# Optimization experiments

Hardware: AMD Instinct MI355X
Metric: run time of the kernel (lower is better)

The kernel has to match this reference:

```python
import jax, jax.numpy as jnp
import numpy as np

B, NN, D = 16, 50, 400
H, DH = 20, 20
ATT_H = 128
NEWS = 20000
K = 10
STEPS, SLOTS = 6, 10
EPS = 1e-5


def _layer_norm(x, g, b):
    m = jnp.mean(x, -1, keepdims=True)
    v = jnp.mean(jnp.square(x - m), -1, keepdims=True)
    return (x - m) * jax.lax.rsqrt(v + EPS) * g + b


def setup_inputs():
    key = jax.random.key(0)
    ks = jax.random.split(key, 9)
    s = 1.0 / np.sqrt(D)
    return {
        "news_input": jax.random.normal(ks[0], (B, NN, D), jnp.float32),
        "outputs_table": jax.random.normal(ks[1], (NEWS, K, D), jnp.float32) * 0.1,
        "Wq": jax.random.normal(ks[2], (D, H * DH), jnp.float32) * s,
        "Wk": jax.random.normal(ks[3], (D, H * DH), jnp.float32) * s,
        "Wv": jax.random.normal(ks[4], (D, H * DH), jnp.float32) * s,
        "ln1_g": jnp.ones((D,), jnp.float32),
        "ln1_b": jnp.zeros((D,), jnp.float32),
        "fc1_w": jax.random.normal(ks[5], (D, ATT_H), jnp.float32) * s,
        "fc1_b": jnp.zeros((ATT_H,), jnp.float32),
        "fc2_w": jax.random.normal(ks[6], (ATT_H, 1), jnp.float32) * (1.0 / np.sqrt(ATT_H)),
        "fc2_b": jnp.zeros((1,), jnp.float32),
        "ln2_g": jnp.ones((D,), jnp.float32),
        "ln2_b": jnp.zeros((D,), jnp.float32),
        "click_history": jax.random.randint(ks[7], (B, NN), 1, NEWS + 1),
        "neighbor_table": jax.random.randint(ks[8], (NEWS + 1, K), 1, NEWS + 1),
        "mask": jnp.ones((B, 50 * SLOTS), jnp.int32),
    }


def _traverse(news_input, outputs_table, click_history, neighbor_table):
    # Vectorized form of the per-item 6-hop neighbor traversal.
    def step(carry, _):
        idx, dead = carry                                          # [B,N] int, [B,N] bool
        vg = outputs_table[idx - 1]                                # [B,N,K,D] gather
        scores = jnp.einsum('bnkd,bnd->bnk', vg, news_input)      # [B,N,K]
        mx_i = jnp.argmax(scores, -1)
        mx_v = jnp.take_along_axis(scores, mx_i[..., None], -1)[..., 0]
        nz = scores != 0
        any_nz = jnp.any(nz, -1)
        nz_i = jnp.argmax(jnp.where(nz, scores, -jnp.inf), -1)
        hop = (mx_v == 0) & jnp.logical_not(dead)                  # max score exactly 0 -> follow graph
        sel_i = jnp.where(hop & any_nz, nz_i, mx_i)
        new_dead = dead | (hop & jnp.logical_not(any_nz))
        nbr = jnp.take_along_axis(neighbor_table[idx], sel_i[..., None], -1)[..., 0]
        new_idx = jnp.where(hop & any_nz, nbr, idx)
        sel = jnp.take_along_axis(vg, sel_i[..., None, None], 2)[..., 0, :]
        sel = jnp.where(new_dead[..., None], 0.0, sel)
        return (new_idx, new_dead), sel

    init = (click_history, jnp.zeros(click_history.shape, bool))
    _, sels = jax.lax.scan(step, init, None, length=STEPS)         # [6,B,N,D]
    sels = jnp.moveaxis(sels, 0, 2)                                # [B,N,6,D]
    valid = jnp.any(news_input != 0, -1).astype(sels.dtype)        # skip all-zero news rows
    sels = sels * valid[..., None, None]
    res = jnp.pad(sels, ((0, 0), (0, 0), (0, SLOTS - STEPS), (0, 0)))
    if NN < 50:
        res = jnp.pad(res, ((0, 0), (0, 50 - NN), (0, 0), (0, 0)))
    return res                                                      # [B,50,10,D]


def _mha(x, mask, Wq, Wk, Wv):
    L = x.shape[1]
    q = (x @ Wq).reshape(-1, L, H, DH).transpose(0, 2, 1, 3)
    k = (x @ Wk).reshape(-1, L, H, DH).transpose(0, 2, 1, 3)
    v = (x @ Wv).reshape(-1, L, H, DH).transpose(0, 2, 1, 3)
    sc = jnp.einsum('bhqd,bhkd->bhqk', q, k) / np.float32(np.sqrt(DH))
    sc = jnp.where(mask[:, None, None, :] > 0, sc, -1e9)
    a = jax.nn.softmax(sc, -1)
    o = jnp.einsum('bhqk,bhkd->bhqd', a, v)
    return o.transpose(0, 2, 1, 3).reshape(-1, L, H * DH)


def _att_pool(x, mask, fc1_w, fc1_b, fc2_w, fc2_b):
    e = jnp.tanh(x @ fc1_w + fc1_b) @ fc2_w + fc2_b                # [B*50,10,1]
    e = jnp.where(mask[..., None] > 0, e, -1e9)
    a = jax.nn.softmax(e, 1)
    return jnp.sum(a * x, 1)


def reference(news_input, outputs_table, Wq, Wk, Wv, ln1_g, ln1_b,
              fc1_w, fc1_b, fc2_w, fc2_b, ln2_g, ln2_b,
              click_history, neighbor_table, mask):
    res = _traverse(news_input, outputs_table, click_history, neighbor_table)
    x = res.reshape(-1, 50 * SLOTS, D)
    x = _mha(x, mask, Wq, Wk, Wv)
    x = x.reshape(-1, SLOTS, D)
    x = _layer_norm(x, ln1_g, ln1_b)
    x = _att_pool(x, mask.reshape(-1, SLOTS), fc1_w, fc1_b, fc2_w, fc2_b)
    x = _layer_norm(x, ln2_g, ln2_b)
    return x.reshape(-1, 50, D)
```

## Files before the change

kernel.cpp:

```cpp
#include <hip/hip_runtime.h>
#include <hip/hip_bf16.h>
#include <math.h>

#define B 16
#define NN 50
#define D 400
#define H 20
#define DH 20
#define ATT_H 128
#define NEWS 20000
#define K 10
#define STEPS 6
#define SLOTS 10
#define L 500
#define EPS 1e-5f

#define XP 416
#define NC 1200

typedef short short4v __attribute__((ext_vector_type(4)));
typedef short short8 __attribute__((ext_vector_type(8)));
typedef float floatx4 __attribute__((ext_vector_type(4)));

__device__ __forceinline__ short f2bf(float f) {
    __hip_bfloat16 h = __float2bfloat16(f);
    return *reinterpret_cast<short*>(&h);
}

__global__ __launch_bounds__(256) void k_traverse(
    const float* __restrict__ news,
    const float* __restrict__ table,
    const int*   __restrict__ click,
    const int*   __restrict__ nbrt,
    short* __restrict__ x)
{
    __shared__ float ssc[K];

    int item = blockIdx.x;
    int b = item / NN, n = item % NN;
    int tid = threadIdx.x;
    int lane = tid & 63, w = tid >> 6;

    float nv[7];
    bool nzf = false;
    #pragma unroll
    for (int i = 0; i < 7; i++) {
        int d = lane + 64 * i;
        float v = (d < D) ? news[(size_t)item * D + d] : 0.0f;
        nv[i] = v;
        nzf |= (v != 0.0f);
    }
    float valid = __any(nzf) ? 1.0f : 0.0f;

    int idx = click[item];
    bool dead = false;
    short* xbase = x + (size_t)(b * L + n * SLOTS) * XP;

    for (int step = 0; step < STEPS; step++) {
        const float* tb = table + (size_t)(idx - 1) * K * D;
        for (int kk = w; kk < K; kk += 4) {
            float p = 0.0f;
            #pragma unroll
            for (int i = 0; i < 7; i++) {
                int d = lane + 64 * i;
                if (d < D) p += tb[kk * D + d] * nv[i];
            }
            #pragma unroll
            for (int off = 32; off > 0; off >>= 1) p += __shfl_xor(p, off);
            if (lane == 0) ssc[kk] = p;
        }
        __syncthreads();

        float scores[K];
        #pragma unroll
        for (int kk = 0; kk < K; kk++) scores[kk] = ssc[kk];

        int mx_i = 0; float mx_v = scores[0];
        #pragma unroll
        for (int kk = 1; kk < K; kk++)
            if (scores[kk] > mx_v) { mx_v = scores[kk]; mx_i = kk; }

        bool any_nz = false; int nz_i = 0; float nz_v = -INFINITY;
        #pragma unroll
        for (int kk = 0; kk < K; kk++) {
            if (scores[kk] != 0.0f) {
                if (!any_nz || scores[kk] > nz_v) { nz_v = scores[kk]; nz_i = kk; }
                any_nz = true;
            }
        }

        bool hop = (mx_v == 0.0f) && !dead;
        int sel_i = (hop && any_nz) ? nz_i : mx_i;
        bool new_dead = dead || (hop && !any_nz);
        int nbr = nbrt[(size_t)idx * K + sel_i];
        int new_idx = (hop && any_nz) ? nbr : idx;

        float scale = new_dead ? 0.0f : valid;
        const float* selrow = tb + (size_t)sel_i * D;
        short* xr = xbase + (size_t)step * XP;
        for (int d = tid; d < XP; d += 256)
            xr[d] = (d < D) ? f2bf(selrow[d] * scale) : (short)0;

        idx = new_idx; dead = new_dead;
        __syncthreads();
    }
    for (int s = STEPS; s < SLOTS; s++) {
        short* xr = xbase + (size_t)s * XP;
        for (int d = tid; d < XP; d += 256) xr[d] = 0;
    }
}

__global__ __launch_bounds__(256) void k_wconvT(
    const float* __restrict__ Wq, const float* __restrict__ Wk,
    const float* __restrict__ Wv, short* __restrict__ wT)
{
    int c = blockIdx.x;
    int z = c / 400, n = c % 400;
    const float* W = (z == 0) ? Wq : (z == 1) ? Wk : Wv;
    for (int k = threadIdx.x; k < XP; k += 256)
        wT[(size_t)c * XP + k] = (k < 400) ? f2bf(W[(size_t)k * 400 + n]) : (short)0;
}

#define BM 128
#define BN 64
#define BKK 32

__global__ __launch_bounds__(256) void k_qkv_mfma(
    const short* __restrict__ xg,
    const short* __restrict__ wT,
    float* __restrict__ c)
{
    __shared__ short xs[BM][BKK + 8];
    __shared__ short wt[BN][BKK + 8];

    int tid = threadIdx.x;
    int m0 = blockIdx.x * BM;
    int n0 = blockIdx.y * BN;
    int lane = tid & 63, w = tid >> 6;
    int wr = w >> 1, wc = w & 1;
    int quad = lane >> 4, l16 = lane & 15;

    floatx4 acc[4][2];
    #pragma unroll
    for (int i = 0; i < 4; i++)
        #pragma unroll
        for (int j = 0; j < 2; j++) acc[i][j] = (floatx4){0.f, 0.f, 0.f, 0.f};

    int xr = tid >> 1, xc = (tid & 1) * 16;
    int wrow = tid >> 2, wcol8 = (tid & 3) * 8;
    bool xok = (m0 + xr) < 8000;
    bool wok = (n0 + wrow) < NC;

    for (int k0 = 0; k0 < XP; k0 += BKK) {
        int4 xv0 = {0,0,0,0}, xv1 = {0,0,0,0}, wv = {0,0,0,0};
        if (xok) {
            const int4* src = (const int4*)(xg + (size_t)(m0 + xr) * XP + k0 + xc);
            xv0 = src[0]; xv1 = src[1];
        }
        if (wok)
            wv = *(const int4*)(wT + (size_t)(n0 + wrow) * XP + k0 + wcol8);
        __syncthreads();
        *(int4*)&xs[xr][xc]      = xv0;
        *(int4*)&xs[xr][xc + 8]  = xv1;
        *(int4*)&wt[wrow][wcol8] = wv;
        __syncthreads();

        short8 a[4], bf[2];
        #pragma unroll
        for (int fi = 0; fi < 4; fi++)
            a[fi] = *(const short8*)&xs[wr * 64 + fi * 16 + l16][quad * 8];
        #pragma unroll
        for (int fj = 0; fj < 2; fj++)
            bf[fj] = *(const short8*)&wt[wc * 32 + fj * 16 + l16][quad * 8];
        #pragma unroll
        for (int fi = 0; fi < 4; fi++)
            #pragma unroll
            for (int fj = 0; fj < 2; fj++)
                acc[fi][fj] = __builtin_amdgcn_mfma_f32_16x16x32_bf16(
                    a[fi], bf[fj], acc[fi][fj], 0, 0, 0);
    }

    #pragma unroll
    for (int fi = 0; fi < 4; fi++) {
        int grow_base = m0 + wr * 64 + fi * 16 + quad * 4;
        #pragma unroll
        for (int fj = 0; fj < 2; fj++) {
            int gcol = n0 + wc * 32 + fj * 16 + l16;
            #pragma unroll
            for (int r = 0; r < 4; r++) {
                int grow = grow_base + r;
                if (grow < 8000 && gcol < NC)
                    c[(size_t)grow * NC + gcol] = acc[fi][fj][r];
            }
        }
    }
}

#define KSTR 24
#define VSTR 520
#define PSTR 40
#define QSPLIT 4

__global__ __launch_bounds__(256) void k_attn4(
    const float* __restrict__ qkv,
    const int* __restrict__ mask,
    float* __restrict__ o)
{
    __shared__ short sh[12288 + 21 * VSTR + 4 * 16 * PSTR + 512];
    short* VTb = sh + 12288;
    short* Pb  = VTb + 21 * VSTR;
    short* msk = Pb + 4 * 16 * PSTR;

    int part = blockIdx.x & (QSPLIT - 1);
    int bh = blockIdx.x >> 2;
    int b = bh / H, h = bh % H;
    int tid = threadIdx.x;
    int lane = tid & 63, w = tid >> 6;
    int quad = lane >> 4, l16 = lane & 15;
    const float scale = 0.22360679774997896f;

    for (int i = tid; i < 512 * KSTR; i += 256) {
        int j = i / KSTR, d = i % KSTR;
        float v = (j < L && d < DH) ? qkv[(size_t)(b * L + j) * NC + 400 + h * DH + d] : 0.0f;
        sh[i] = f2bf(v);
    }
    for (int i = tid; i < L * DH; i += 256) {
        int j = i / DH, d = i % DH;
        VTb[d * VSTR + j] = f2bf(qkv[(size_t)(b * L + j) * NC + 800 + h * DH + d]);
    }
    for (int j = tid; j < 512; j += 256) {
        VTb[20 * VSTR + j] = (j < L) ? f2bf(1.0f) : (short)0;
        msk[j] = (j < L && mask[(size_t)b * L + j] > 0) ? f2bf(1.0f) : (short)0;
    }
    for (int i = tid; i < DH * 12; i += 256) {
        int d = i / 12, j = L + i % 12;
        VTb[d * VSTR + j] = 0;
    }
    __syncthreads();

    short* Pw = Pb + w * 16 * PSTR;
    short* pwr = Pw + l16 * PSTR;
    const short* prd = Pw + l16 * PSTR + quad * 8;
    const short* kA  = sh + quad * 8;
    const short* vA0 = VTb + l16 * VSTR;
    int r1 = 16 + l16; if (r1 > 20) r1 = 20;
    const short* vA1 = VTb + r1 * VSTR;

    for (int qt = part * 8 + w; qt < part * 8 + 8; qt += 4) {
        int qrow = qt * 16 + l16;
        const float* qp = qkv + (size_t)(b * L + (qrow < L ? qrow : 0)) * NC + h * DH;
        short8 aq;
        #pragma unroll
        for (int jj = 0; jj < 8; jj++) {
            int k = quad * 8 + jj;
            float v = (k < DH) ? qp[k] * scale : 0.0f;
            aq[jj] = f2bf(v);
        }

        floatx4 O0 = (floatx4){0.f,0.f,0.f,0.f};
        floatx4 O1 = (floatx4){0.f,0.f,0.f,0.f};
        float mrun = -INFINITY;

        for (int jt = 0; jt < 16; jt++) {
            short8 ak0 = (short8)(short)0, ak1 = (short8)(short)0;
            if (quad < 3) {
                ak0 = *(const short8*)&kA[(jt * 32 + l16) * KSTR];
                ak1 = *(const short8*)&kA[(jt * 32 + 16 + l16) * KSTR];
            }
            floatx4 z = (floatx4){0.f,0.f,0.f,0.f};
            floatx4 s0 = __builtin_amdgcn_mfma_f32_16x16x32_bf16(ak0, aq, z, 0, 0, 0);
            floatx4 s1 = __builtin_amdgcn_mfma_f32_16x16x32_bf16(ak1, aq, z, 0, 0, 0);

            short4v mk0 = *(const short4v*)&msk[jt * 32 + quad * 4];
            short4v mk1 = *(const short4v*)&msk[jt * 32 + 16 + quad * 4];
            #pragma unroll
            for (int r = 0; r < 4; r++) {
                s0[r] = (mk0[r] != 0) ? s0[r] : -1e9f;
                s1[r] = (mk1[r] != 0) ? s1[r] : -1e9f;
            }

            float mt = fmaxf(fmaxf(fmaxf(s0[0], s0[1]), fmaxf(s0[2], s0[3])),
                             fmaxf(fmaxf(s1[0], s1[1]), fmaxf(s1[2], s1[3])));
            mt = fmaxf(mt, __shfl_xor(mt, 16));
            mt = fmaxf(mt, __shfl_xor(mt, 32));

            if (!__all(mt <= mrun)) {
                float mnew = fmaxf(mrun, mt);
                float alpha = __expf(mrun - mnew);
                mrun = mnew;
                #pragma unroll
                for (int r = 0; r < 4; r++) { O0[r] *= alpha; O1[r] *= alpha; }
            }

            short4v pk0, pk1;
            #pragma unroll
            for (int r = 0; r < 4; r++) {
                pk0[r] = f2bf(__expf(s0[r] - mrun));
                pk1[r] = f2bf(__expf(s1[r] - mrun));
            }
            *(short4v*)&pwr[quad * 4]      = pk0;
            *(short4v*)&pwr[16 + quad * 4] = pk1;

            short8 ap  = *(const short8*)prd;
            short8 va0 = *(const short8*)&vA0[jt * 32 + quad * 8];
            short8 va1 = *(const short8*)&vA1[jt * 32 + quad * 8];
            O0 = __builtin_amdgcn_mfma_f32_16x16x32_bf16(va0, ap, O0, 0, 0, 0);
            O1 = __builtin_amdgcn_mfma_f32_16x16x32_bf16(va1, ap, O1, 0, 0, 0);
        }

        float lsum = __shfl(O1[0], 16 + l16);
        float inv = 1.0f / lsum;
        int q = qt * 16 + l16;
        if (q < L) {
            float* op = o + (size_t)(b * L + q) * (H * DH) + h * DH;
            floatx4 v0;
            #pragma unroll
            for (int r = 0; r < 4; r++) v0[r] = O0[r] * inv;
            *(floatx4*)&op[quad * 4] = v0;
            if (quad == 0) {
                floatx4 v1;
                #pragma unroll
                for (int r = 0; r < 4; r++) v1[r] = O1[r] * inv;
                *(floatx4*)&op[16] = v1;
            }
        }
    }
}

__global__ __launch_bounds__(256) void k_pool(
    const float* __restrict__ o,
    const float* __restrict__ ln1g, const float* __restrict__ ln1b,
    const float* __restrict__ fc1w, const float* __restrict__ fc1b,
    const float* __restrict__ fc2w, const float* __restrict__ fc2b,
    const float* __restrict__ ln2g, const float* __restrict__ ln2b,
    const int* __restrict__ mask,
    float* __restrict__ out)
{
    __shared__ float xt[SLOTS][D];
    __shared__ float hv[SLOTS * ATT_H];
    __shared__ float es[SLOTS];
    __shared__ float red[8];

    int g = blockIdx.x;
    int tid = threadIdx.x;
    int lane = tid & 63, w = tid >> 6;

    const float* xg = o + (size_t)g * SLOTS * D;

    for (int s = w; s < SLOTS; s += 4) {
        const float* xr = xg + (size_t)s * D;
        float vbuf[7];
        float sum = 0.0f, sq = 0.0f;
        #pragma unroll
        for (int i = 0; i < 7; i++) {
            int d = lane + 64 * i;
            float v = (d < D) ? xr[d] : 0.0f;
            vbuf[i] = v; sum += v; sq += v * v;
        }
        #pragma unroll
        for (int off = 32; off > 0; off >>= 1) {
            sum += __shfl_xor(sum, off);
            sq  += __shfl_xor(sq, off);
        }
        float mean = sum / (float)D;
        float var = sq / (float)D - mean * mean;
        float rs = rsqrtf(var + EPS);
        #pragma unroll
        for (int i = 0; i < 7; i++) {
            int d = lane + 64 * i;
            if (d < D) xt[s][d] = (vbuf[i] - mean) * rs * ln1g[d] + ln1b[d];
        }
    }
    __syncthreads();

    {
        int jh = tid & 127;
        int s0 = tid >> 7;
        float hs[5];
        #pragma unroll
        for (int jj = 0; jj < 5; jj++) hs[jj] = fc1b[jh];
        for (int d = 0; d < D; d++) {
            float fw = fc1w[(size_t)d * ATT_H + jh];
            #pragma unroll
            for (int jj = 0; jj < 5; jj++) hs[jj] += xt[s0 + 2 * jj][d] * fw;
        }
        float f2 = fc2w[jh];
        #pragma unroll
        for (int jj = 0; jj < 5; jj++)
            hv[(s0 + 2 * jj) * ATT_H + jh] = tanhf(hs[jj]) * f2;
    }
    __syncthreads();

    for (int s = w; s < SLOTS; s += 4) {
        float p = hv[s * ATT_H + lane] + hv[s * ATT_H + lane + 64];
        #pragma unroll
        for (int off = 32; off > 0; off >>= 1) p += __shfl_xor(p, off);
        if (lane == 0) es[s] = p + fc2b[0];
    }
    __syncthreads();

    float ev[SLOTS];
    float emax = -INFINITY;
    #pragma unroll
    for (int s = 0; s < SLOTS; s++) {
        float e = (mask[(size_t)g * SLOTS + s] > 0) ? es[s] : -1e9f;
        ev[s] = e;
        if (e > emax) emax = e;
    }
    float esum = 0.0f;
    #pragma unroll
    for (int s = 0; s < SLOTS; s++) { ev[s] = __expf(ev[s] - emax); esum += ev[s]; }
    float einv = 1.0f / esum;

    int d0 = tid, d1 = tid + 256;
    float p0 = 0.0f, p1 = 0.0f;
    #pragma unroll
    for (int s = 0; s < SLOTS; s++) {
        p0 += ev[s] * xt[s][d0];
        if (d1 < D) p1 += ev[s] * xt[s][d1];
    }
    p0 *= einv; p1 *= einv;

    float sum = p0 + ((d1 < D) ? p1 : 0.0f);
    float sq  = p0 * p0 + ((d1 < D) ? p1 * p1 : 0.0f);
    #pragma unroll
    for (int off = 32; off > 0; off >>= 1) {
        sum += __shfl_xor(sum, off);
        sq  += __shfl_xor(sq, off);
    }
    if (lane == 0) { red[w] = sum; red[4 + w] = sq; }
    __syncthreads();
    float tsum = red[0] + red[1] + red[2] + red[3];
    float tsq  = red[4] + red[5] + red[6] + red[7];
    float mean = tsum / (float)D;
    float var = tsq / (float)D - mean * mean;
    float rs = rsqrtf(var + EPS);

    float* og = out + (size_t)g * D;
    og[d0] = (p0 - mean) * rs * ln2g[d0] + ln2b[d0];
    if (d1 < D) og[d1] = (p1 - mean) * rs * ln2g[d1] + ln2b[d1];
}

extern "C" void kernel_launch(void* const* d_in, const int* in_sizes, int n_in,
                              void* d_out, int out_size, void* d_ws, size_t ws_size,
                              hipStream_t stream) {
    const float* news  = (const float*)d_in[0];
    const float* table = (const float*)d_in[1];
    const float* Wq    = (const float*)d_in[2];
    const float* Wk    = (const float*)d_in[3];
    const float* Wv    = (const float*)d_in[4];
    const float* ln1g  = (const float*)d_in[5];
    const float* ln1b  = (const float*)d_in[6];
    const float* fc1w  = (const float*)d_in[7];
    const float* fc1b  = (const float*)d_in[8];
    const float* fc2w  = (const float*)d_in[9];
    const float* fc2b  = (const float*)d_in[10];
    const float* ln2g  = (const float*)d_in[11];
    const float* ln2b  = (const float*)d_in[12];
    const int* click   = (const int*)d_in[13];
    const int* nbrt    = (const int*)d_in[14];
    const int* mask    = (const int*)d_in[15];
    float* out = (float*)d_out;

    char* p = (char*)d_ws;
    short* xbf = (short*)p;  p += (size_t)8000 * XP * sizeof(short);
    short* wT  = (short*)p;  p += (size_t)NC * XP * sizeof(short);
    float* qkv = (float*)p;  p += (size_t)8000 * NC * sizeof(float);
    float* ob  = (float*)p;

    k_traverse<<<dim3(B * NN), dim3(256), 0, stream>>>(news, table, click, nbrt, xbf);
    k_wconvT<<<dim3(NC), dim3(256), 0, stream>>>(Wq, Wk, Wv, wT);
    k_qkv_mfma<<<dim3((8000 + BM - 1) / BM, (NC + BN - 1) / BN), dim3(256), 0, stream>>>(
        xbf, wT, qkv);
    k_attn4<<<dim3(B * H * QSPLIT), dim3(256), 0, stream>>>(qkv, mask, ob);
    k_pool<<<dim3(B * NN), dim3(256), 0, stream>>>(ob, ln1g, ln1b, fc1w, fc1b, fc2w, fc2b,
                                                   ln2g, ln2b, mask, out);
}
```

Baseline: 551.4 us.

## Store QKV in bf16, fold query scale into Wq, merge prep kernels

The QKV projection now writes bf16 instead of fp32, which halves the intermediate buffer traffic between the GEMM and the attention kernel and removes the per-load conversions in attention. The 1/sqrt(DH) query scale is folded into the transposed Wq during weight conversion. The traversal and weight-transpose kernels are merged into one launch. Rounding Q/K/V to bf16 before storage matches what attention already did after loading, so accuracy should be about the same. The only difference is that the scale is now applied before rounding.

```diff
diff --git a/kernel.cpp b/kernel.cpp
--- a/kernel.cpp
+++ b/kernel.cpp
@@ -27,18 +27,33 @@
     return *reinterpret_cast<short*>(&h);
 }
 
-__global__ __launch_bounds__(256) void k_traverse(
+__global__ __launch_bounds__(256) void k_prep(
     const float* __restrict__ news,
     const float* __restrict__ table,
     const int*   __restrict__ click,
     const int*   __restrict__ nbrt,
-    short* __restrict__ x)
+    const float* __restrict__ Wq, const float* __restrict__ Wk,
+    const float* __restrict__ Wv,
+    short* __restrict__ x,
+    short* __restrict__ wT)
 {
     __shared__ float ssc[K];
 
-    int item = blockIdx.x;
+    int blk = blockIdx.x;
+    int tid = threadIdx.x;
+
+    if (blk >= B * NN) {
+        int c = blk - B * NN;
+        int z = c / 400, n = c % 400;
+        const float* W = (z == 0) ? Wq : (z == 1) ? Wk : Wv;
+        float sc = (z == 0) ? 0.22360679774997896f : 1.0f;
+        for (int k = tid; k < XP; k += 256)
+            wT[(size_t)c * XP + k] = (k < 400) ? f2bf(W[(size_t)k * 400 + n] * sc) : (short)0;
+        return;
+    }
+
+    int item = blk;
     int b = item / NN, n = item % NN;
-    int tid = threadIdx.x;
     int lane = tid & 63, w = tid >> 6;
 
     float nv[7];
@@ -110,17 +125,6 @@
     }
 }
 
-__global__ __launch_bounds__(256) void k_wconvT(
-    const float* __restrict__ Wq, const float* __restrict__ Wk,
-    const float* __restrict__ Wv, short* __restrict__ wT)
-{
-    int c = blockIdx.x;
-    int z = c / 400, n = c % 400;
-    const float* W = (z == 0) ? Wq : (z == 1) ? Wk : Wv;
-    for (int k = threadIdx.x; k < XP; k += 256)
-        wT[(size_t)c * XP + k] = (k < 400) ? f2bf(W[(size_t)k * 400 + n]) : (short)0;
-}
-
 #define BM 128
 #define BN 64
 #define BKK 32
@@ -128,7 +132,7 @@
 __global__ __launch_bounds__(256) void k_qkv_mfma(
     const short* __restrict__ xg,
     const short* __restrict__ wT,
-    float* __restrict__ c)
+    short* __restrict__ c)
 {
     __shared__ short xs[BM][BKK + 8];
     __shared__ short wt[BN][BKK + 8];
@@ -190,7 +194,7 @@
             for (int r = 0; r < 4; r++) {
                 int grow = grow_base + r;
                 if (grow < 8000 && gcol < NC)
-                    c[(size_t)grow * NC + gcol] = acc[fi][fj][r];
+                    c[(size_t)grow * NC + gcol] = f2bf(acc[fi][fj][r]);
             }
         }
     }
@@ -202,7 +206,7 @@
 #define QSPLIT 4
 
 __global__ __launch_bounds__(256) void k_attn4(
-    const float* __restrict__ qkv,
+    const short* __restrict__ qkv,
     const int* __restrict__ mask,
     float* __restrict__ o)
 {
@@ -217,16 +221,15 @@
     int tid = threadIdx.x;
     int lane = tid & 63, w = tid >> 6;
     int quad = lane >> 4, l16 = lane & 15;
-    const float scale = 0.22360679774997896f;
 
     for (int i = tid; i < 512 * KSTR; i += 256) {
         int j = i / KSTR, d = i % KSTR;
-        float v = (j < L && d < DH) ? qkv[(size_t)(b * L + j) * NC + 400 + h * DH + d] : 0.0f;
-        sh[i] = f2bf(v);
+        sh[i] = (j < L && d < DH) ? qkv[(size_t)(b * L + j) * NC + 400 + h * DH + d]
+                                  : (short)0;
     }
     for (int i = tid; i < L * DH; i += 256) {
         int j = i / DH, d = i % DH;
-        VTb[d * VSTR + j] = f2bf(qkv[(size_t)(b * L + j) * NC + 800 + h * DH + d]);
+        VTb[d * VSTR + j] = qkv[(size_t)(b * L + j) * NC + 800 + h * DH + d];
     }
     for (int j = tid; j < 512; j += 256) {
         VTb[20 * VSTR + j] = (j < L) ? f2bf(1.0f) : (short)0;
@@ -248,13 +251,12 @@
 
     for (int qt = part * 8 + w; qt < part * 8 + 8; qt += 4) {
         int qrow = qt * 16 + l16;
-        const float* qp = qkv + (size_t)(b * L + (qrow < L ? qrow : 0)) * NC + h * DH;
+        const short* qp = qkv + (size_t)(b * L + (qrow < L ? qrow : 0)) * NC + h * DH;
         short8 aq;
         #pragma unroll
         for (int jj = 0; jj < 8; jj++) {
             int k = quad * 8 + jj;
-            float v = (k < DH) ? qp[k] * scale : 0.0f;
-            aq[jj] = f2bf(v);
+            aq[jj] = (qrow < L && k < DH) ? qp[k] : (short)0;
         }
 
         floatx4 O0 = (floatx4){0.f,0.f,0.f,0.f};
@@ -465,11 +467,11 @@
     char* p = (char*)d_ws;
     short* xbf = (short*)p;  p += (size_t)8000 * XP * sizeof(short);
     short* wT  = (short*)p;  p += (size_t)NC * XP * sizeof(short);
-    float* qkv = (float*)p;  p += (size_t)8000 * NC * sizeof(float);
+    short* qkv = (short*)p;  p += (size_t)8000 * NC * sizeof(short);
     float* ob  = (float*)p;
 
-    k_traverse<<<dim3(B * NN), dim3(256), 0, stream>>>(news, table, click, nbrt, xbf);
-    k_wconvT<<<dim3(NC), dim3(256), 0, stream>>>(Wq, Wk, Wv, wT);
+    k_prep<<<dim3(B * NN + NC), dim3(256), 0, stream>>>(
+        news, table, click, nbrt, Wq, Wk, Wv, xbf, wT);
     k_qkv_mfma<<<dim3((8000 + BM - 1) / BM, (NC + BN - 1) / BN), dim3(256), 0, stream>>>(
         xbf, wT, qkv);
     k_attn4<<<dim3(B * H * QSPLIT), dim3(256), 0, stream>>>(qkv, mask, ob);
```

Result: no change. 542.1 us (-1.7%).
